# Optimization experiments

Hardware: AMD Instinct MI355X
Metric: run time of the kernel (lower is better)

The kernel has to match this reference:

```python
import jax, jax.numpy as jnp
import numpy as np

TAU_MEM = 20.0
TAU_SYN = 5.0
ALPHA_MEM = float(np.exp(-1.0 / TAU_MEM))
ALPHA_SYN = float(np.exp(-1.0 / TAU_SYN))
CONNECTIVITY = 0.1
SPECTRAL_RADIUS = 0.9


def setup_inputs() -> dict:
    key = jax.random.key(0)
    k1, k2, k3, k4 = jax.random.split(key, 4)
    B, D, N = 2048, 256, 512
    rates = jax.random.normal(k1, (B, D), dtype=jnp.float32)
    input_weight = jax.random.normal(k2, (N, D), dtype=jnp.float32) * 0.1
    W = jax.random.normal(k3, (N, N), dtype=jnp.float32)
    mask = (jax.random.uniform(k4, (N, N)) < CONNECTIVITY).astype(jnp.float32)
    W = W * mask
    # mirror torch init: scale by spectral_radius / max eigvalsh
    max_eig = jnp.linalg.eigvalsh(W)[-1]
    W = W * (SPECTRAL_RADIUS / max_eig)
    return {
        "rates": rates,
        "input_weight": input_weight,
        "reservoir_weight": W,
        "v_mem": jnp.zeros((B, N), dtype=jnp.float32),
        "current": jnp.zeros((B, N), dtype=jnp.float32),
        "n_steps": 64,
    }


def reference(rates, input_weight, reservoir_weight, v_mem, current, n_steps):
    dtype = rates.dtype
    # input current is identical every step in the original loop -> hoist it
    input_current = rates @ input_weight.T  # (B, N)

    def step(carry, _):
        v, c, spike_sum = carry
        rec = (c > 0).astype(dtype) @ reservoir_weight  # (B, N)
        c = ALPHA_SYN * c + (1.0 - ALPHA_SYN) * (input_current + rec)
        v = ALPHA_MEM * v + (1.0 - ALPHA_MEM) * c
        spike_sum = spike_sum + (v > 0).astype(dtype)
        return (v, c, spike_sum), None

    (v, c, spike_sum), _ = jax.lax.scan(
        step, (v_mem, current, jnp.zeros_like(v_mem)), None, length=n_steps
    )
    readout = spike_sum / n_steps  # == stack(spikes).mean(dim=1)
    return readout, (v, c)
```

## Files before the change

### kernel.cpp

```cpp
#include <hip/hip_runtime.h>
#include <stdint.h>


#define N_NEU 512
#define B_ROWS 2048
#define D_IN 256
#define R_PB 8
#define NBLK (B_ROWS / R_PB)

#define WS_PERM    0
#define WS_RANK    2048
#define WS_CNT     4096
#define WS_CNTW    8192
#define WS_IBASE   8256
#define WS_WBASE   8320
#define WS_IDX     16384
#define WS_WT      81920

#define SPK_OFF(k)  ((k) << 4)
#define SPK_BUF     8192

#define H16_ONE 0x3C00u
#define MAXPB   32

__global__ __launch_bounds__(256) void lsm_count(
    const float* __restrict__ W, uint32_t* __restrict__ ws)
{
    int t  = threadIdx.x;
    int k0 = blockIdx.x * 4;
    int c0 = 0, c1 = 0;
    #pragma unroll
    for (int kk = 0; kk < 4; ++kk) {
        const float* row = W + (size_t)(k0 + kk) * N_NEU;
        c0 += (row[t]       != 0.0f) ? 1 : 0;
        c1 += (row[t + 256] != 0.0f) ? 1 : 0;
    }
    if (c0) atomicAdd(&ws[(WS_CNT >> 2) + t],       (uint32_t)c0);
    if (c1) atomicAdd(&ws[(WS_CNT >> 2) + t + 256], (uint32_t)c1);
}

__global__ __launch_bounds__(512) void lsm_sort(uint32_t* __restrict__ ws)
{
    __shared__ int hist[N_NEU + 1];
    __shared__ int csort[N_NEU];
    __shared__ int gcw[8];

    int t = threadIdx.x;
    int creal = (int)ws[(WS_CNT >> 2) + t];
    for (int i = t; i < N_NEU + 1; i += 512) hist[i] = 0;
    __syncthreads();
    atomicAdd(&hist[creal], 1);
    __syncthreads();
    if (t == 0) {
        int acc = 0;
        for (int v = 0; v <= N_NEU; ++v) { int h = hist[v]; hist[v] = acc; acc += h; }
    }
    __syncthreads();
    int rank = atomicAdd(&hist[creal], 1);
    ws[(WS_PERM >> 2) + rank] = (uint32_t)t;
    ws[(WS_RANK >> 2) + t]    = (uint32_t)rank;
    csort[rank] = creal;
    __syncthreads();
    if (t < 8) {
        int cw = csort[t * 64 + 63];
        cw = (cw + 7) & ~7;
        gcw[t] = cw;
        ws[(WS_CNTW >> 2) + t] = (uint32_t)cw;
    }
    __syncthreads();
    if (t == 0) {
        int ai = 0, aw = 0;
        for (int g = 0; g < 8; ++g) {
            ws[(WS_IBASE >> 2) + g] = (uint32_t)ai;
            ws[(WS_WBASE >> 2) + g] = (uint32_t)aw;
            ai += gcw[g] * 64 * 2;
            aw += gcw[g] * 64 * 4;
        }
    }
}

__global__ __launch_bounds__(64) void lsm_fill(
    const float* __restrict__ W, uint32_t* __restrict__ ws)
{
    int c    = blockIdx.x;
    int lane = threadIdx.x;
    char* base = (char*)ws;

    uint32_t rank = ws[(WS_RANK >> 2) + c];
    int ls = (int)(rank & 63), g = (int)(rank >> 6);
    int cw = (int)ws[(WS_CNTW >> 2) + g];
    uint32_t ib = ws[(WS_IBASE >> 2) + g];
    uint32_t wb = ws[(WS_WBASE >> 2) + g];

    __shared__ unsigned short ent_k[8][MAXPB];
    __shared__ float          ent_w[8][MAXPB];
    __shared__ int            nb[8];

    int bm = lane & 7;
    unsigned long long mbk   = 0x0101010101010101ULL << bm;
    unsigned long long below = (1ULL << lane) - 1;
    int myBase = 0;
    for (int i = 0; i < 8; ++i) {
        int k = lane + 64 * i;
        float wv = W[(size_t)k * N_NEU + c];
        bool nz = (wv != 0.0f);
        unsigned long long bal = __ballot(nz);
        if (nz) {
            int p = myBase + __popcll(bal & mbk & below);
            ent_k[bm][p] = (unsigned short)k;
            ent_w[bm][p] = wv;
        }
        myBase += __popcll(bal & mbk);
    }
    if (lane < 8) nb[lane] = myBase;
    __syncthreads();

    int Q = cw >> 3;
    for (int j = lane; j < cw; j += 64) {
        int b = (j + ls) & 7;
        int m = j >> 3;
        int nbb = nb[b];
        int d = (nbb < Q) ? nbb : Q;
        unsigned short kk; float wv;
        if (m < d) {
            kk = ent_k[b][m]; wv = ent_w[b][m];
        } else {
            int f = m - d;
            for (int bp = 0; bp < b; ++bp) {
                int nn = nb[bp];
                f += (Q > nn) ? (Q - nn) : 0;
            }
            int acc = 0, bsel = -1, isel = 0;
            for (int bp = 0; bp < 8; ++bp) {
                int ov = nb[bp] - Q; ov = (ov > 0) ? ov : 0;
                if (bsel < 0 && f < acc + ov) { bsel = bp; isel = Q + (f - acc); }
                acc += ov;
            }
            if (bsel >= 0) { kk = ent_k[bsel][isel]; wv = ent_w[bsel][isel]; }
            else           { kk = (unsigned short)b; wv = 0.0f; }
        }
        *(unsigned short*)(base + WS_IDX + ib + (j >> 3) * 1024 + ls * 16 + (j & 7) * 2)
            = (unsigned short)SPK_OFF(kk);
        *(float*)(base + WS_WT + wb + (j >> 3) * 2048 + ls * 32 + (j & 7) * 4) = wv;
    }
}

#define GATH(P, X, B) \
    P##0 = *(const uint4*)((B) + ((X).x & 0xffffu)); \
    P##1 = *(const uint4*)((B) + ((X).x >> 16));     \
    P##2 = *(const uint4*)((B) + ((X).y & 0xffffu)); \
    P##3 = *(const uint4*)((B) + ((X).y >> 16));     \
    P##4 = *(const uint4*)((B) + ((X).z & 0xffffu)); \
    P##5 = *(const uint4*)((B) + ((X).z >> 16));     \
    P##6 = *(const uint4*)((B) + ((X).w & 0xffffu)); \
    P##7 = *(const uint4*)((B) + ((X).w >> 16));

#define FMIX_LO(ACC, WV, S) \
    asm("v_fma_mix_f32 %0, %1, %2, %0 op_sel:[0,0,0] op_sel_hi:[0,1,0]" \
        : "+v"(ACC) : "v"(WV), "v"(S));
#define FMIX_HI(ACC, WV, S) \
    asm("v_fma_mix_f32 %0, %1, %2, %0 op_sel:[0,1,0] op_sel_hi:[0,1,0]" \
        : "+v"(ACC) : "v"(WV), "v"(S));

#define C1(S, WV) \
    FMIX_LO(rec0, WV, (S).x) FMIX_HI(rec1, WV, (S).x) \
    FMIX_LO(rec2, WV, (S).y) FMIX_HI(rec3, WV, (S).y) \
    FMIX_LO(rec4, WV, (S).z) FMIX_HI(rec5, WV, (S).z) \
    FMIX_LO(rec6, WV, (S).w) FMIX_HI(rec7, WV, (S).w)

#define CONS(P, WA, WB) \
    C1(P##0, (WA).x) C1(P##1, (WA).y) C1(P##2, (WA).z) C1(P##3, (WA).w) \
    C1(P##4, (WB).x) C1(P##5, (WB).y) C1(P##6, (WB).z) C1(P##7, (WB).w)

#define LDW(WA, WB, K) \
    WA = ((const float4*)(wp0 + (K) * 2048))[0]; \
    WB = ((const float4*)(wp0 + (K) * 2048))[1];

#define CHUNK(K, X) \
    if ((K) < nw) { LDW(waA, wbA, K)  GATH(a, X, sb)  CONS(a, waA, wbA) }

__global__ __launch_bounds__(1024, 4)
void lsm_main(
    const float* __restrict__ rates, const float* __restrict__ inW,
    const float* __restrict__ vin,   const float* __restrict__ cin,
    const int* __restrict__ nsteps_p,
    const uint32_t* __restrict__ ws, float* __restrict__ out)
{
    __shared__ __align__(16) unsigned char smem[2 * SPK_BUF + 16384 + 16384];
    float* stg  = (float*)(smem + 2 * SPK_BUF);
    float* rl   = stg;
    float* pbuf = (float*)(smem + 2 * SPK_BUF + 16384);

    int q    = threadIdx.x;
    int blk  = blockIdx.x;
    int r0   = blk * R_PB;
    int w    = q >> 6;
    int lane = q & 63;
    int half = w >> 3;
    int wp   = w & 7;
    int wg   = (wp < 4) ? wp : (11 - wp);
    int n    = (int)ws[(WS_PERM >> 2) + wg * 64 + lane];
    int cw   = (int)ws[(WS_CNTW >> 2) + wg];
    int nit  = cw >> 3;
    int nh   = (nit + 1) >> 1;
    int nw   = half ? (nit - nh) : nh;
    const char* ip0 = (const char*)ws + WS_IDX + ws[(WS_IBASE >> 2) + wg]
                    + lane * 16 + (half ? nh * 1024 : 0);
    const char* wp0 = (const char*)ws + WS_WT  + ws[(WS_WBASE >> 2) + wg]
                    + lane * 32 + (half ? nh * 2048 : 0);
    int spk_n = SPK_OFF(n);
    float* pb = pbuf + wg * 512 + lane;

    float c0v[R_PB], v0v[R_PB];
    for (int i = q; i < R_PB * N_NEU; i += 1024)
        stg[i] = cin[(size_t)r0 * N_NEU + i];
    __syncthreads();
    if (!half) {
        #pragma unroll
        for (int r = 0; r < R_PB; ++r) c0v[r] = stg[r * N_NEU + n];
    }
    __syncthreads();
    for (int i = q; i < R_PB * N_NEU; i += 1024)
        stg[i] = vin[(size_t)r0 * N_NEU + i];
    __syncthreads();
    if (!half) {
        #pragma unroll
        for (int r = 0; r < R_PB; ++r) v0v[r] = stg[r * N_NEU + n];
    }
    __syncthreads();

    if (q < (R_PB * D_IN) / 4)
        ((float4*)rl)[q] = ((const float4*)(rates + (size_t)r0 * D_IN))[q];
    __syncthreads();

    float I[R_PB] = {0.f, 0.f, 0.f, 0.f, 0.f, 0.f, 0.f, 0.f};
    if (!half) {
        const float4* wrow = (const float4*)(inW + (size_t)n * D_IN);
        for (int d4 = 0; d4 < D_IN / 4; ++d4) {
            float4 wv = wrow[d4];
            #pragma unroll
            for (int r = 0; r < R_PB; ++r) {
                const float* rr = rl + r * D_IN + d4 * 4;
                I[r] += wv.x * rr[0] + wv.y * rr[1] + wv.z * rr[2] + wv.w * rr[3];
            }
        }
        uint4 sini = make_uint4(0u, 0u, 0u, 0u);
        #pragma unroll
        for (int r = 0; r < R_PB; ++r) {
            unsigned hb = (c0v[r] > 0.f) ? H16_ONE : 0u;
            unsigned sh = (r & 1) ? 16 : 0;
            if (r < 2)      sini.x |= hb << sh;
            else if (r < 4) sini.y |= hb << sh;
            else if (r < 6) sini.z |= hb << sh;
            else            sini.w |= hb << sh;
        }
        *(uint4*)(smem + spk_n) = sini;
    }

    unsigned ssx = 0u, ssy = 0u;

    uint4 xr0, xr1, xr2, xr3, xr4, xr5;
    const uint4 xz = make_uint4(0u, 0u, 0u, 0u);
    xr0 = (0 < nw) ? *(const uint4*)(ip0)        : xz;
    xr1 = (1 < nw) ? *(const uint4*)(ip0 + 1024) : xz;
    xr2 = (2 < nw) ? *(const uint4*)(ip0 + 2048) : xz;
    xr3 = (3 < nw) ? *(const uint4*)(ip0 + 3072) : xz;
    xr4 = (4 < nw) ? *(const uint4*)(ip0 + 4096) : xz;
    xr5 = (5 < nw) ? *(const uint4*)(ip0 + 5120) : xz;

    const float AS   = (float)0.8187307530779818;
    const float OMAS = (float)(1.0 - 0.8187307530779818);
    const float AM   = (float)0.9512294245007140;
    const float OMAM = (float)(1.0 - 0.9512294245007140);

    int T = nsteps_p[0];
    __syncthreads();

    #pragma unroll 1
    for (int t = 0; t < T; ++t) {
        const unsigned char* sb = smem + ((t & 1) ? SPK_BUF : 0);
        unsigned char*       db = smem + ((t & 1) ? 0 : SPK_BUF);

        float rec0 = 0.f, rec1 = 0.f, rec2 = 0.f, rec3 = 0.f;
        float rec4 = 0.f, rec5 = 0.f, rec6 = 0.f, rec7 = 0.f;
        uint4 a0, a1, a2, a3, a4, a5, a6, a7;
        float4 waA, wbA;

        CHUNK(0, xr0)
        CHUNK(1, xr1)
        CHUNK(2, xr2)
        CHUNK(3, xr3)
        CHUNK(4, xr4)
        CHUNK(5, xr5)

        if (half) {
            pb[0]   = rec0; pb[64]  = rec1; pb[128] = rec2; pb[192] = rec3;
            pb[256] = rec4; pb[320] = rec5; pb[384] = rec6; pb[448] = rec7;
        }
        __syncthreads();

        if (!half) {
            rec0 += pb[0];   rec1 += pb[64];  rec2 += pb[128]; rec3 += pb[192];
            rec4 += pb[256]; rec5 += pb[320]; rec6 += pb[384]; rec7 += pb[448];

            uint4 ns = make_uint4(0u, 0u, 0u, 0u);
            unsigned vbx = 0u, vby = 0u;
            {
                float rca[R_PB] = {rec0, rec1, rec2, rec3, rec4, rec5, rec6, rec7};
                #pragma unroll
                for (int r = 0; r < R_PB; ++r) {
                    c0v[r] = AS * c0v[r] + OMAS * (I[r] + rca[r]);
                    v0v[r] = AM * v0v[r] + OMAM * c0v[r];
                    unsigned hb = (c0v[r] > 0.f) ? H16_ONE : 0u;
                    unsigned vb = (v0v[r] > 0.f) ? 1u : 0u;
                    unsigned sh = (r & 1) ? 16 : 0;
                    if (r < 2)      ns.x |= hb << sh;
                    else if (r < 4) ns.y |= hb << sh;
                    else if (r < 6) ns.z |= hb << sh;
                    else            ns.w |= hb << sh;
                    if (r < 4) vbx |= vb << (r * 8);
                    else       vby |= vb << ((r - 4) * 8);
                }
            }
            ssx += vbx;
            ssy += vby;
            *(uint4*)(db + spk_n) = ns;
        }
        __syncthreads();
    }

    float invT = 1.0f / (float)T;
    size_t BN = (size_t)B_ROWS * N_NEU;

    if (!half) {
        #pragma unroll
        for (int r = 0; r < R_PB; ++r) {
            unsigned cnt = (r < 4) ? ((ssx >> (r * 8)) & 0xffu)
                                   : ((ssy >> ((r - 4) * 8)) & 0xffu);
            stg[r * N_NEU + n] = (float)cnt * invT;
        }
    }
    __syncthreads();
    for (int i = q; i < R_PB * N_NEU; i += 1024)
        out[(size_t)r0 * N_NEU + i] = stg[i];
    __syncthreads();

    if (!half) {
        #pragma unroll
        for (int r = 0; r < R_PB; ++r) stg[r * N_NEU + n] = v0v[r];
    }
    __syncthreads();
    for (int i = q; i < R_PB * N_NEU; i += 1024)
        out[BN + (size_t)r0 * N_NEU + i] = stg[i];
    __syncthreads();

    if (!half) {
        #pragma unroll
        for (int r = 0; r < R_PB; ++r) stg[r * N_NEU + n] = c0v[r];
    }
    __syncthreads();
    for (int i = q; i < R_PB * N_NEU; i += 1024)
        out[2 * BN + (size_t)r0 * N_NEU + i] = stg[i];
}

extern "C" void kernel_launch(void* const* d_in, const int* in_sizes, int n_in,
                              void* d_out, int out_size, void* d_ws, size_t ws_size,
                              hipStream_t stream)
{
    const float* rates = (const float*)d_in[0];
    const float* inW   = (const float*)d_in[1];
    const float* W     = (const float*)d_in[2];
    const float* vin   = (const float*)d_in[3];
    const float* cin   = (const float*)d_in[4];
    const int*   nst   = (const int*)d_in[5];
    uint32_t* ws = (uint32_t*)d_ws;
    float* out = (float*)d_out;
    (void)in_sizes; (void)n_in; (void)out_size; (void)ws_size;

    hipMemsetAsync((char*)d_ws + WS_CNT, 0, 2048, stream);

    lsm_count<<<128, 256, 0, stream>>>(W, ws);
    lsm_sort<<<1, 512, 0, stream>>>(ws);
    lsm_fill<<<N_NEU, 64, 0, stream>>>(W, ws);
    lsm_main<<<NBLK, 1024, 0, stream>>>(rates, inW, vin, cin, nst, ws, out);
}
```

Before: 306.3 us.

## Store spikes as bytes, use ubyte-convert FMAs, transpose W for coalesced fill

Spike state in shared memory moves from half-precision pairs (16 bytes per neuron) to one byte per row (8 bytes per neuron). Gathers become 8-byte loads and the FMA uses v_cvt_f32_ubyte plus v_fmac instead of v_fma_mix. This halves LDS gather traffic at the cost of extra convert instructions. The count kernel also writes a transposed copy of W into the output buffer so the fill kernel reads coalesced rows. The bucket count in fill becomes 16, which changes padding to multiples of 16.

```diff
diff --git a/kernel.cpp b/kernel.cpp
--- a/kernel.cpp
+++ b/kernel.cpp
@@ -17,23 +17,27 @@
 #define WS_IDX     16384
 #define WS_WT      81920
 
-#define SPK_OFF(k)  ((k) << 4)
-#define SPK_BUF     8192
-
-#define H16_ONE 0x3C00u
-#define MAXPB   32
-
-__global__ __launch_bounds__(256) void lsm_count(
-    const float* __restrict__ W, uint32_t* __restrict__ ws)
+#define SPK_OFF(k)  ((k) << 3)
+#define SPK_BUF     4096
+
+#define MAXPB   24
+
+__global__ __launch_bounds__(256) void lsm_count_tr(
+    const float* __restrict__ W, uint32_t* __restrict__ ws,
+    float* __restrict__ wT)
 {
     int t  = threadIdx.x;
-    int k0 = blockIdx.x * 4;
+    int k0 = blockIdx.x * 2;
     int c0 = 0, c1 = 0;
     #pragma unroll
-    for (int kk = 0; kk < 4; ++kk) {
+    for (int kk = 0; kk < 2; ++kk) {
         const float* row = W + (size_t)(k0 + kk) * N_NEU;
-        c0 += (row[t]       != 0.0f) ? 1 : 0;
-        c1 += (row[t + 256] != 0.0f) ? 1 : 0;
+        float a = row[t];
+        float b = row[t + 256];
+        wT[(size_t)t * N_NEU + k0 + kk]         = a;
+        wT[(size_t)(t + 256) * N_NEU + k0 + kk] = b;
+        c0 += (a != 0.0f) ? 1 : 0;
+        c1 += (b != 0.0f) ? 1 : 0;
     }
     if (c0) atomicAdd(&ws[(WS_CNT >> 2) + t],       (uint32_t)c0);
     if (c1) atomicAdd(&ws[(WS_CNT >> 2) + t + 256], (uint32_t)c1);
@@ -63,7 +67,7 @@
     __syncthreads();
     if (t < 8) {
         int cw = csort[t * 64 + 63];
-        cw = (cw + 7) & ~7;
+        cw = (cw + 15) & ~15;
         gcw[t] = cw;
         ws[(WS_CNTW >> 2) + t] = (uint32_t)cw;
     }
@@ -80,7 +84,7 @@
 }
 
 __global__ __launch_bounds__(64) void lsm_fill(
-    const float* __restrict__ W, uint32_t* __restrict__ ws)
+    const float* __restrict__ wT, uint32_t* __restrict__ ws)
 {
     int c    = blockIdx.x;
     int lane = threadIdx.x;
@@ -92,17 +96,17 @@
     uint32_t ib = ws[(WS_IBASE >> 2) + g];
     uint32_t wb = ws[(WS_WBASE >> 2) + g];
 
-    __shared__ unsigned short ent_k[8][MAXPB];
-    __shared__ float          ent_w[8][MAXPB];
-    __shared__ int            nb[8];
-
-    int bm = lane & 7;
-    unsigned long long mbk   = 0x0101010101010101ULL << bm;
+    __shared__ unsigned short ent_k[16][MAXPB];
+    __shared__ float          ent_w[16][MAXPB];
+    __shared__ int            nb[16];
+
+    int bm = lane & 15;
+    unsigned long long mbk   = 0x0001000100010001ULL << bm;
     unsigned long long below = (1ULL << lane) - 1;
     int myBase = 0;
     for (int i = 0; i < 8; ++i) {
         int k = lane + 64 * i;
-        float wv = W[(size_t)k * N_NEU + c];
+        float wv = wT[(size_t)c * N_NEU + k];
         bool nz = (wv != 0.0f);
         unsigned long long bal = __ballot(nz);
         if (nz) {
@@ -112,13 +116,13 @@
         }
         myBase += __popcll(bal & mbk);
     }
-    if (lane < 8) nb[lane] = myBase;
-    __syncthreads();
-
-    int Q = cw >> 3;
+    if (lane < 16) nb[lane] = myBase;
+    __syncthreads();
+
+    int Q = cw >> 4;
     for (int j = lane; j < cw; j += 64) {
-        int b = (j + ls) & 7;
-        int m = j >> 3;
+        int b = (j + ls) & 15;
+        int m = j >> 4;
         int nbb = nb[b];
         int d = (nbb < Q) ? nbb : Q;
         unsigned short kk; float wv;
@@ -131,7 +135,7 @@
                 f += (Q > nn) ? (Q - nn) : 0;
             }
             int acc = 0, bsel = -1, isel = 0;
-            for (int bp = 0; bp < 8; ++bp) {
+            for (int bp = 0; bp < 16; ++bp) {
                 int ov = nb[bp] - Q; ov = (ov > 0) ? ov : 0;
                 if (bsel < 0 && f < acc + ov) { bsel = bp; isel = Q + (f - acc); }
                 acc += ov;
@@ -146,27 +150,28 @@
 }
 
 #define GATH(P, X, B) \
-    P##0 = *(const uint4*)((B) + ((X).x & 0xffffu)); \
-    P##1 = *(const uint4*)((B) + ((X).x >> 16));     \
-    P##2 = *(const uint4*)((B) + ((X).y & 0xffffu)); \
-    P##3 = *(const uint4*)((B) + ((X).y >> 16));     \
-    P##4 = *(const uint4*)((B) + ((X).z & 0xffffu)); \
-    P##5 = *(const uint4*)((B) + ((X).z >> 16));     \
-    P##6 = *(const uint4*)((B) + ((X).w & 0xffffu)); \
-    P##7 = *(const uint4*)((B) + ((X).w >> 16));
-
-#define FMIX_LO(ACC, WV, S) \
-    asm("v_fma_mix_f32 %0, %1, %2, %0 op_sel:[0,0,0] op_sel_hi:[0,1,0]" \
-        : "+v"(ACC) : "v"(WV), "v"(S));
-#define FMIX_HI(ACC, WV, S) \
-    asm("v_fma_mix_f32 %0, %1, %2, %0 op_sel:[0,1,0] op_sel_hi:[0,1,0]" \
-        : "+v"(ACC) : "v"(WV), "v"(S));
-
-#define C1(S, WV) \
-    FMIX_LO(rec0, WV, (S).x) FMIX_HI(rec1, WV, (S).x) \
-    FMIX_LO(rec2, WV, (S).y) FMIX_HI(rec3, WV, (S).y) \
-    FMIX_LO(rec4, WV, (S).z) FMIX_HI(rec5, WV, (S).z) \
-    FMIX_LO(rec6, WV, (S).w) FMIX_HI(rec7, WV, (S).w)
+    P##0 = *(const uint2*)((B) + ((X).x & 0xffffu)); \
+    P##1 = *(const uint2*)((B) + ((X).x >> 16));     \
+    P##2 = *(const uint2*)((B) + ((X).y & 0xffffu)); \
+    P##3 = *(const uint2*)((B) + ((X).y >> 16));     \
+    P##4 = *(const uint2*)((B) + ((X).z & 0xffffu)); \
+    P##5 = *(const uint2*)((B) + ((X).z >> 16));     \
+    P##6 = *(const uint2*)((B) + ((X).w & 0xffffu)); \
+    P##7 = *(const uint2*)((B) + ((X).w >> 16));
+
+#define CV0(F, M) asm("v_cvt_f32_ubyte0 %0, %1" : "=v"(F) : "v"(M));
+#define CV1(F, M) asm("v_cvt_f32_ubyte1 %0, %1" : "=v"(F) : "v"(M));
+#define CV2(F, M) asm("v_cvt_f32_ubyte2 %0, %1" : "=v"(F) : "v"(M));
+#define CV3(F, M) asm("v_cvt_f32_ubyte3 %0, %1" : "=v"(F) : "v"(M));
+#define FMC(ACC, WV, F) \
+    asm("v_fmac_f32 %0, %1, %2" : "+v"(ACC) : "v"(WV), "v"(F));
+
+#define C1(S, WV) { \
+    float f0, f1, f2, f3, f4, f5, f6, f7; \
+    CV0(f0, (S).x) CV1(f1, (S).x) CV2(f2, (S).x) CV3(f3, (S).x) \
+    CV0(f4, (S).y) CV1(f5, (S).y) CV2(f6, (S).y) CV3(f7, (S).y) \
+    FMC(rec0, WV, f0) FMC(rec1, WV, f1) FMC(rec2, WV, f2) FMC(rec3, WV, f3) \
+    FMC(rec4, WV, f4) FMC(rec5, WV, f5) FMC(rec6, WV, f6) FMC(rec7, WV, f7) }
 
 #define CONS(P, WA, WB) \
     C1(P##0, (WA).x) C1(P##1, (WA).y) C1(P##2, (WA).z) C1(P##3, (WA).w) \
@@ -244,17 +249,14 @@
                 I[r] += wv.x * rr[0] + wv.y * rr[1] + wv.z * rr[2] + wv.w * rr[3];
             }
         }
-        uint4 sini = make_uint4(0u, 0u, 0u, 0u);
+        uint2 sini = make_uint2(0u, 0u);
         #pragma unroll
         for (int r = 0; r < R_PB; ++r) {
-            unsigned hb = (c0v[r] > 0.f) ? H16_ONE : 0u;
-            unsigned sh = (r & 1) ? 16 : 0;
-            if (r < 2)      sini.x |= hb << sh;
-            else if (r < 4) sini.y |= hb << sh;
-            else if (r < 6) sini.z |= hb << sh;
-            else            sini.w |= hb << sh;
-        }
-        *(uint4*)(smem + spk_n) = sini;
+            unsigned hb = (c0v[r] > 0.f) ? 1u : 0u;
+            if (r < 4) sini.x |= hb << (r * 8);
+            else       sini.y |= hb << ((r - 4) * 8);
+        }
+        *(uint2*)(smem + spk_n) = sini;
     }
 
     unsigned ssx = 0u, ssy = 0u;
@@ -283,7 +285,7 @@
 
         float rec0 = 0.f, rec1 = 0.f, rec2 = 0.f, rec3 = 0.f;
         float rec4 = 0.f, rec5 = 0.f, rec6 = 0.f, rec7 = 0.f;
-        uint4 a0, a1, a2, a3, a4, a5, a6, a7;
+        uint2 a0, a1, a2, a3, a4, a5, a6, a7;
         float4 waA, wbA;
 
         CHUNK(0, xr0)
@@ -303,7 +305,7 @@
             rec0 += pb[0];   rec1 += pb[64];  rec2 += pb[128]; rec3 += pb[192];
             rec4 += pb[256]; rec5 += pb[320]; rec6 += pb[384]; rec7 += pb[448];
 
-            uint4 ns = make_uint4(0u, 0u, 0u, 0u);
+            uint2 ns = make_uint2(0u, 0u);
             unsigned vbx = 0u, vby = 0u;
             {
                 float rca[R_PB] = {rec0, rec1, rec2, rec3, rec4, rec5, rec6, rec7};
@@ -311,20 +313,15 @@
                 for (int r = 0; r < R_PB; ++r) {
                     c0v[r] = AS * c0v[r] + OMAS * (I[r] + rca[r]);
                     v0v[r] = AM * v0v[r] + OMAM * c0v[r];
-                    unsigned hb = (c0v[r] > 0.f) ? H16_ONE : 0u;
+                    unsigned hb = (c0v[r] > 0.f) ? 1u : 0u;
                     unsigned vb = (v0v[r] > 0.f) ? 1u : 0u;
-                    unsigned sh = (r & 1) ? 16 : 0;
-                    if (r < 2)      ns.x |= hb << sh;
-                    else if (r < 4) ns.y |= hb << sh;
-                    else if (r < 6) ns.z |= hb << sh;
-                    else            ns.w |= hb << sh;
-                    if (r < 4) vbx |= vb << (r * 8);
-                    else       vby |= vb << ((r - 4) * 8);
+                    if (r < 4) { ns.x |= hb << (r * 8);       vbx |= vb << (r * 8); }
+                    else       { ns.y |= hb << ((r - 4) * 8); vby |= vb << ((r - 4) * 8); }
                 }
             }
             ssx += vbx;
             ssy += vby;
-            *(uint4*)(db + spk_n) = ns;
+            *(uint2*)(db + spk_n) = ns;
         }
         __syncthreads();
     }
@@ -377,10 +374,12 @@
     float* out = (float*)d_out;
     (void)in_sizes; (void)n_in; (void)out_size; (void)ws_size;
 
+    float* wT = out;
+
     hipMemsetAsync((char*)d_ws + WS_CNT, 0, 2048, stream);
 
-    lsm_count<<<128, 256, 0, stream>>>(W, ws);
+    lsm_count_tr<<<256, 256, 0, stream>>>(W, ws, wT);
     lsm_sort<<<1, 512, 0, stream>>>(ws);
-    lsm_fill<<<N_NEU, 64, 0, stream>>>(W, ws);
+    lsm_fill<<<N_NEU, 64, 0, stream>>>(wT, ws);
     lsm_main<<<NBLK, 1024, 0, stream>>>(rates, inW, vin, cin, nst, ws, out);
 }
```

Result: slower. 363.4 us (+18.6%).

## Split neuron work across wave halves and merge via permlane swap

Applied to the files above, without the earlier changes.

Each wave now handles 32 neurons, with its two 32-lane halves each covering half of the sparse-row chunks. The two partial sums are combined with v_permlane32_swap instead of going through a shared-memory buffer and an extra block barrier, so the LDS pbuf and one __syncthreads per step disappear. Neurons are now grouped in 16 groups of 32. The count kernel also writes a transposed copy of W into the output buffer, which makes the fill kernel's column reads coalesced. In exchange, the input-current and LIF update math now runs redundantly in both half-waves, and the scratch transpose relies on lsm_main later overwriting the output region.

```diff
diff --git a/kernel.cpp b/kernel.cpp
--- a/kernel.cpp
+++ b/kernel.cpp
@@ -23,17 +23,22 @@
 #define H16_ONE 0x3C00u
 #define MAXPB   32
 
-__global__ __launch_bounds__(256) void lsm_count(
-    const float* __restrict__ W, uint32_t* __restrict__ ws)
+__global__ __launch_bounds__(256) void lsm_count_tr(
+    const float* __restrict__ W, uint32_t* __restrict__ ws,
+    float* __restrict__ wT)
 {
     int t  = threadIdx.x;
-    int k0 = blockIdx.x * 4;
+    int k0 = blockIdx.x * 2;
     int c0 = 0, c1 = 0;
     #pragma unroll
-    for (int kk = 0; kk < 4; ++kk) {
+    for (int kk = 0; kk < 2; ++kk) {
         const float* row = W + (size_t)(k0 + kk) * N_NEU;
-        c0 += (row[t]       != 0.0f) ? 1 : 0;
-        c1 += (row[t + 256] != 0.0f) ? 1 : 0;
+        float a = row[t];
+        float b = row[t + 256];
+        wT[(size_t)t * N_NEU + k0 + kk]         = a;
+        wT[(size_t)(t + 256) * N_NEU + k0 + kk] = b;
+        c0 += (a != 0.0f) ? 1 : 0;
+        c1 += (b != 0.0f) ? 1 : 0;
     }
     if (c0) atomicAdd(&ws[(WS_CNT >> 2) + t],       (uint32_t)c0);
     if (c1) atomicAdd(&ws[(WS_CNT >> 2) + t + 256], (uint32_t)c1);
@@ -43,7 +48,7 @@
 {
     __shared__ int hist[N_NEU + 1];
     __shared__ int csort[N_NEU];
-    __shared__ int gcw[8];
+    __shared__ int gcw[16];
 
     int t = threadIdx.x;
     int creal = (int)ws[(WS_CNT >> 2) + t];
@@ -61,8 +66,8 @@
     ws[(WS_RANK >> 2) + t]    = (uint32_t)rank;
     csort[rank] = creal;
     __syncthreads();
-    if (t < 8) {
-        int cw = csort[t * 64 + 63];
+    if (t < 16) {
+        int cw = csort[t * 32 + 31];
         cw = (cw + 7) & ~7;
         gcw[t] = cw;
         ws[(WS_CNTW >> 2) + t] = (uint32_t)cw;
@@ -70,24 +75,24 @@
     __syncthreads();
     if (t == 0) {
         int ai = 0, aw = 0;
-        for (int g = 0; g < 8; ++g) {
+        for (int g = 0; g < 16; ++g) {
             ws[(WS_IBASE >> 2) + g] = (uint32_t)ai;
             ws[(WS_WBASE >> 2) + g] = (uint32_t)aw;
-            ai += gcw[g] * 64 * 2;
-            aw += gcw[g] * 64 * 4;
+            ai += gcw[g] * 32 * 2;
+            aw += gcw[g] * 32 * 4;
         }
     }
 }
 
 __global__ __launch_bounds__(64) void lsm_fill(
-    const float* __restrict__ W, uint32_t* __restrict__ ws)
+    const float* __restrict__ wT, uint32_t* __restrict__ ws)
 {
     int c    = blockIdx.x;
     int lane = threadIdx.x;
     char* base = (char*)ws;
 
     uint32_t rank = ws[(WS_RANK >> 2) + c];
-    int ls = (int)(rank & 63), g = (int)(rank >> 6);
+    int ls32 = (int)(rank & 31), g = (int)(rank >> 5);
     int cw = (int)ws[(WS_CNTW >> 2) + g];
     uint32_t ib = ws[(WS_IBASE >> 2) + g];
     uint32_t wb = ws[(WS_WBASE >> 2) + g];
@@ -102,7 +107,7 @@
     int myBase = 0;
     for (int i = 0; i < 8; ++i) {
         int k = lane + 64 * i;
-        float wv = W[(size_t)k * N_NEU + c];
+        float wv = wT[(size_t)c * N_NEU + k];
         bool nz = (wv != 0.0f);
         unsigned long long bal = __ballot(nz);
         if (nz) {
@@ -117,7 +122,7 @@
 
     int Q = cw >> 3;
     for (int j = lane; j < cw; j += 64) {
-        int b = (j + ls) & 7;
+        int b = (j + ls32) & 7;
         int m = j >> 3;
         int nbb = nb[b];
         int d = (nbb < Q) ? nbb : Q;
@@ -139,9 +144,9 @@
             if (bsel >= 0) { kk = ent_k[bsel][isel]; wv = ent_w[bsel][isel]; }
             else           { kk = (unsigned short)b; wv = 0.0f; }
         }
-        *(unsigned short*)(base + WS_IDX + ib + (j >> 3) * 1024 + ls * 16 + (j & 7) * 2)
+        *(unsigned short*)(base + WS_IDX + ib + (j >> 3) * 512 + ls32 * 16 + (j & 7) * 2)
             = (unsigned short)SPK_OFF(kk);
-        *(float*)(base + WS_WT + wb + (j >> 3) * 2048 + ls * 32 + (j & 7) * 4) = wv;
+        *(float*)(base + WS_WT + wb + (j >> 3) * 1024 + ls32 * 32 + (j & 7) * 4) = wv;
     }
 }
 
@@ -173,11 +178,16 @@
     C1(P##4, (WB).x) C1(P##5, (WB).y) C1(P##6, (WB).z) C1(P##7, (WB).w)
 
 #define LDW(WA, WB, K) \
-    WA = ((const float4*)(wp0 + (K) * 2048))[0]; \
-    WB = ((const float4*)(wp0 + (K) * 2048))[1];
+    WA = ((const float4*)(wp0 + (K) * 1024))[0]; \
+    WB = ((const float4*)(wp0 + (K) * 1024))[1];
 
 #define CHUNK(K, X) \
     if ((K) < nw) { LDW(waA, wbA, K)  GATH(a, X, sb)  CONS(a, waA, wbA) }
+
+#define MERGE(R) { \
+    float _y = R; \
+    asm("v_permlane32_swap_b32 %0, %1" : "+v"(R), "+v"(_y)); \
+    R = R + _y; }
 
 __global__ __launch_bounds__(1024, 4)
 void lsm_main(
@@ -186,47 +196,40 @@
     const int* __restrict__ nsteps_p,
     const uint32_t* __restrict__ ws, float* __restrict__ out)
 {
-    __shared__ __align__(16) unsigned char smem[2 * SPK_BUF + 16384 + 16384];
+    __shared__ __align__(16) unsigned char smem[2 * SPK_BUF + 16384];
     float* stg  = (float*)(smem + 2 * SPK_BUF);
     float* rl   = stg;
-    float* pbuf = (float*)(smem + 2 * SPK_BUF + 16384);
 
     int q    = threadIdx.x;
     int blk  = blockIdx.x;
     int r0   = blk * R_PB;
     int w    = q >> 6;
     int lane = q & 63;
-    int half = w >> 3;
-    int wp   = w & 7;
-    int wg   = (wp < 4) ? wp : (11 - wp);
-    int n    = (int)ws[(WS_PERM >> 2) + wg * 64 + lane];
-    int cw   = (int)ws[(WS_CNTW >> 2) + wg];
+    int ls32 = lane & 31;
+    int hs   = lane >> 5;
+    int n    = (int)ws[(WS_PERM >> 2) + w * 32 + ls32];
+    int cw   = (int)ws[(WS_CNTW >> 2) + w];
     int nit  = cw >> 3;
     int nh   = (nit + 1) >> 1;
-    int nw   = half ? (nit - nh) : nh;
-    const char* ip0 = (const char*)ws + WS_IDX + ws[(WS_IBASE >> 2) + wg]
-                    + lane * 16 + (half ? nh * 1024 : 0);
-    const char* wp0 = (const char*)ws + WS_WT  + ws[(WS_WBASE >> 2) + wg]
-                    + lane * 32 + (half ? nh * 2048 : 0);
+    int nw   = hs ? (nit - nh) : nh;
+    const char* ip0 = (const char*)ws + WS_IDX + ws[(WS_IBASE >> 2) + w]
+                    + ls32 * 16 + (hs ? nh * 512 : 0);
+    const char* wp0 = (const char*)ws + WS_WT  + ws[(WS_WBASE >> 2) + w]
+                    + ls32 * 32 + (hs ? nh * 1024 : 0);
     int spk_n = SPK_OFF(n);
-    float* pb = pbuf + wg * 512 + lane;
 
     float c0v[R_PB], v0v[R_PB];
     for (int i = q; i < R_PB * N_NEU; i += 1024)
         stg[i] = cin[(size_t)r0 * N_NEU + i];
     __syncthreads();
-    if (!half) {
-        #pragma unroll
-        for (int r = 0; r < R_PB; ++r) c0v[r] = stg[r * N_NEU + n];
-    }
+    #pragma unroll
+    for (int r = 0; r < R_PB; ++r) c0v[r] = stg[r * N_NEU + n];
     __syncthreads();
     for (int i = q; i < R_PB * N_NEU; i += 1024)
         stg[i] = vin[(size_t)r0 * N_NEU + i];
     __syncthreads();
-    if (!half) {
-        #pragma unroll
-        for (int r = 0; r < R_PB; ++r) v0v[r] = stg[r * N_NEU + n];
-    }
+    #pragma unroll
+    for (int r = 0; r < R_PB; ++r) v0v[r] = stg[r * N_NEU + n];
     __syncthreads();
 
     if (q < (R_PB * D_IN) / 4)
@@ -234,7 +237,7 @@
     __syncthreads();
 
     float I[R_PB] = {0.f, 0.f, 0.f, 0.f, 0.f, 0.f, 0.f, 0.f};
-    if (!half) {
+    {
         const float4* wrow = (const float4*)(inW + (size_t)n * D_IN);
         for (int d4 = 0; d4 < D_IN / 4; ++d4) {
             float4 wv = wrow[d4];
@@ -244,6 +247,9 @@
                 I[r] += wv.x * rr[0] + wv.y * rr[1] + wv.z * rr[2] + wv.w * rr[3];
             }
         }
+    }
+
+    if (lane < 32) {
         uint4 sini = make_uint4(0u, 0u, 0u, 0u);
         #pragma unroll
         for (int r = 0; r < R_PB; ++r) {
@@ -262,11 +268,11 @@
     uint4 xr0, xr1, xr2, xr3, xr4, xr5;
     const uint4 xz = make_uint4(0u, 0u, 0u, 0u);
     xr0 = (0 < nw) ? *(const uint4*)(ip0)        : xz;
-    xr1 = (1 < nw) ? *(const uint4*)(ip0 + 1024) : xz;
-    xr2 = (2 < nw) ? *(const uint4*)(ip0 + 2048) : xz;
-    xr3 = (3 < nw) ? *(const uint4*)(ip0 + 3072) : xz;
-    xr4 = (4 < nw) ? *(const uint4*)(ip0 + 4096) : xz;
-    xr5 = (5 < nw) ? *(const uint4*)(ip0 + 5120) : xz;
+    xr1 = (1 < nw) ? *(const uint4*)(ip0 + 512)  : xz;
+    xr2 = (2 < nw) ? *(const uint4*)(ip0 + 1024) : xz;
+    xr3 = (3 < nw) ? *(const uint4*)(ip0 + 1536) : xz;
+    xr4 = (4 < nw) ? *(const uint4*)(ip0 + 2048) : xz;
+    xr5 = (5 < nw) ? *(const uint4*)(ip0 + 2560) : xz;
 
     const float AS   = (float)0.8187307530779818;
     const float OMAS = (float)(1.0 - 0.8187307530779818);
@@ -293,46 +299,38 @@
         CHUNK(4, xr4)
         CHUNK(5, xr5)
 
-        if (half) {
-            pb[0]   = rec0; pb[64]  = rec1; pb[128] = rec2; pb[192] = rec3;
-            pb[256] = rec4; pb[320] = rec5; pb[384] = rec6; pb[448] = rec7;
-        }
-        __syncthreads();
-
-        if (!half) {
-            rec0 += pb[0];   rec1 += pb[64];  rec2 += pb[128]; rec3 += pb[192];
-            rec4 += pb[256]; rec5 += pb[320]; rec6 += pb[384]; rec7 += pb[448];
-
-            uint4 ns = make_uint4(0u, 0u, 0u, 0u);
-            unsigned vbx = 0u, vby = 0u;
-            {
-                float rca[R_PB] = {rec0, rec1, rec2, rec3, rec4, rec5, rec6, rec7};
-                #pragma unroll
-                for (int r = 0; r < R_PB; ++r) {
-                    c0v[r] = AS * c0v[r] + OMAS * (I[r] + rca[r]);
-                    v0v[r] = AM * v0v[r] + OMAM * c0v[r];
-                    unsigned hb = (c0v[r] > 0.f) ? H16_ONE : 0u;
-                    unsigned vb = (v0v[r] > 0.f) ? 1u : 0u;
-                    unsigned sh = (r & 1) ? 16 : 0;
-                    if (r < 2)      ns.x |= hb << sh;
-                    else if (r < 4) ns.y |= hb << sh;
-                    else if (r < 6) ns.z |= hb << sh;
-                    else            ns.w |= hb << sh;
-                    if (r < 4) vbx |= vb << (r * 8);
-                    else       vby |= vb << ((r - 4) * 8);
-                }
+        MERGE(rec0) MERGE(rec1) MERGE(rec2) MERGE(rec3)
+        MERGE(rec4) MERGE(rec5) MERGE(rec6) MERGE(rec7)
+
+        uint4 ns = make_uint4(0u, 0u, 0u, 0u);
+        unsigned vbx = 0u, vby = 0u;
+        {
+            float rca[R_PB] = {rec0, rec1, rec2, rec3, rec4, rec5, rec6, rec7};
+            #pragma unroll
+            for (int r = 0; r < R_PB; ++r) {
+                c0v[r] = AS * c0v[r] + OMAS * (I[r] + rca[r]);
+                v0v[r] = AM * v0v[r] + OMAM * c0v[r];
+                unsigned hb = (c0v[r] > 0.f) ? H16_ONE : 0u;
+                unsigned vb = (v0v[r] > 0.f) ? 1u : 0u;
+                unsigned sh = (r & 1) ? 16 : 0;
+                if (r < 2)      ns.x |= hb << sh;
+                else if (r < 4) ns.y |= hb << sh;
+                else if (r < 6) ns.z |= hb << sh;
+                else            ns.w |= hb << sh;
+                if (r < 4) vbx |= vb << (r * 8);
+                else       vby |= vb << ((r - 4) * 8);
             }
-            ssx += vbx;
-            ssy += vby;
-            *(uint4*)(db + spk_n) = ns;
-        }
+        }
+        ssx += vbx;
+        ssy += vby;
+        if (lane < 32) *(uint4*)(db + spk_n) = ns;
         __syncthreads();
     }
 
     float invT = 1.0f / (float)T;
     size_t BN = (size_t)B_ROWS * N_NEU;
 
-    if (!half) {
+    if (lane < 32) {
         #pragma unroll
         for (int r = 0; r < R_PB; ++r) {
             unsigned cnt = (r < 4) ? ((ssx >> (r * 8)) & 0xffu)
@@ -345,7 +343,7 @@
         out[(size_t)r0 * N_NEU + i] = stg[i];
     __syncthreads();
 
-    if (!half) {
+    if (lane < 32) {
         #pragma unroll
         for (int r = 0; r < R_PB; ++r) stg[r * N_NEU + n] = v0v[r];
     }
@@ -354,7 +352,7 @@
         out[BN + (size_t)r0 * N_NEU + i] = stg[i];
     __syncthreads();
 
-    if (!half) {
+    if (lane < 32) {
         #pragma unroll
         for (int r = 0; r < R_PB; ++r) stg[r * N_NEU + n] = c0v[r];
     }
@@ -377,10 +375,12 @@
     float* out = (float*)d_out;
     (void)in_sizes; (void)n_in; (void)out_size; (void)ws_size;
 
+    float* wT = out;
+
     hipMemsetAsync((char*)d_ws + WS_CNT, 0, 2048, stream);
 
-    lsm_count<<<128, 256, 0, stream>>>(W, ws);
+    lsm_count_tr<<<256, 256, 0, stream>>>(W, ws, wT);
     lsm_sort<<<1, 512, 0, stream>>>(ws);
-    lsm_fill<<<N_NEU, 64, 0, stream>>>(W, ws);
+    lsm_fill<<<N_NEU, 64, 0, stream>>>(wT, ws);
     lsm_main<<<NBLK, 1024, 0, stream>>>(rates, inW, vin, cin, nst, ws, out);
 }
```

Result: slower. 338.1 us (+10.4%).
